# Kernel tuning notes

Measured on AMD Instinct MI355X. Metric: run time of the kernel, lower is better.

Reference implementation:

```python
import jax, jax.numpy as jnp
import numpy as np

L, E, TOP_K = 3, 8, 2
B, N, D, DS = 256, 1024, 512, 128

def setup_inputs() -> dict:
    key = jax.random.key(0)
    ks = jax.random.split(key, 10)
    s = 0.05  # weight init scale
    return {
        "token": jax.random.normal(ks[0], (B, 1, D), jnp.float32),
        "node_emb": jax.random.normal(ks[1], (B, N, D), jnp.float32),
        "states": jnp.zeros((L, E, B, DS), jnp.float32),
        "Wg": jax.random.normal(ks[2], (L, D, E), jnp.float32) * s,
        "bg": jnp.zeros((L, E), jnp.float32),
        "A": jax.random.normal(ks[3], (L, E, DS), jnp.float32),
        "Bin": jax.random.normal(ks[4], (L, E, D, DS), jnp.float32) * s,
        "Cout": jax.random.normal(ks[5], (L, E, DS, D), jnp.float32) * s,
        "Dsk": jax.random.normal(ks[6], (L, E, D), jnp.float32) * s,
        "Wq": jax.random.normal(ks[7], (D, D), jnp.float32) * s,
        "bq": jnp.zeros((D,), jnp.float32),
    }

def reference(token, node_emb, states, Wg, bg, A, Bin, Cout, Dsk, Wq, bq):
    # token: (B,1,D) -> h: (B,D)
    h = token[:, 0, :]
    lb_loss = jnp.float32(0.0)
    new_states = []
    for l in range(L):
        # --- MoE router: top-k softmax gating ---
        probs = jax.nn.softmax(h @ Wg[l] + bg[l])              # (B,E)
        topv, topi = jax.lax.top_k(probs, TOP_K)               # (B,k)
        gates_k = topv / jnp.sum(topv, axis=-1, keepdims=True)  # renormalized
        oh = jax.nn.one_hot(topi, E, dtype=probs.dtype)        # (B,k,E)
        gate_full = jnp.einsum('bk,bke->be', gates_k, oh)      # (B,E)
        sel = jnp.sum(oh, axis=1) > 0                          # (B,E) bool
        # --- state-space experts (computed densely for all experts) ---
        s = states[l]                                          # (E,B,DS)
        decay = jax.nn.sigmoid(A[l])[:, None, :]               # (E,1,DS)
        s_new = decay * s + jnp.einsum('bd,eds->ebs', h, Bin[l])   # (E,B,DS)
        y = jnp.einsum('ebs,esd->ebd', s_new, Cout[l]) + h[None] * Dsk[l][:, None, :]
        out = jnp.einsum('be,ebd->bd', gate_full, y)           # weighted combine
        # only routed experts advance their state
        keep = sel.T[:, :, None]                               # (E,B,1)
        new_states.append(jnp.where(keep, s_new, s))
        # load-balance loss: E * sum_e mean(probs_e) * mean(frac routed to e)
        lb_loss = lb_loss + E * jnp.sum(jnp.mean(probs, axis=0) * jnp.mean(sel.astype(probs.dtype), axis=0))
        h = h + out                                            # residual
    # --- query projection + logits over nodes ---
    q = h @ Wq + bq                                            # (B,D)
    logits = jnp.einsum('bd,bnd->bn', q, node_emb) / jnp.sqrt(jnp.float32(D))
    return logits, jnp.stack(new_states), lb_loss
```

## Files before the change

### kernel.cpp

```cpp
#include <hip/hip_runtime.h>
#include <math.h>

#define LNUM 3
#define ENUM 8
#define TOPK 2
#define BSZ 256
#define NSZ 1024
#define DSZ 512
#define SSZ 128

typedef float f32x4 __attribute__((ext_vector_type(4)));

__global__ __launch_bounds__(1024, 2) void fused_kernel(
    const float* __restrict__ token,
    const float* __restrict__ states,
    const float* __restrict__ Wg,
    const float* __restrict__ bg,
    const float* __restrict__ A,
    const float* __restrict__ Bin,
    const float* __restrict__ Cout,
    const float* __restrict__ Dsk,
    const float* __restrict__ Wq,
    const float* __restrict__ bq,
    float* __restrict__ out_states,
    float* __restrict__ acc,
    float* __restrict__ q_out)
{
    const int b = blockIdx.x;
    const int t = threadIdx.x;
    const int wave = t >> 6;
    const int lane = t & 63;
    const int ehalf = t >> 9;

    __shared__ float h_s[DSZ];
    __shared__ float snew_s[TOPK][SSZ];
    __shared__ float logit_s[ENUM];
    __shared__ f32x4 part4[1024];
    float* part = (float*)part4;

    if (t < DSZ) h_s[t] = token[b * DSZ + t];

    for (int l = 0; l < LNUM; ++l) {
        const float* Wg_l  = Wg  + (size_t)l * DSZ * ENUM;
        const float* bg_l  = bg  + (size_t)l * ENUM;
        const float* A_l   = A   + (size_t)l * ENUM * SSZ;
        const float* Bin_l = Bin + (size_t)l * ENUM * DSZ * SSZ;
        const float* Cou_l = Cout+ (size_t)l * ENUM * SSZ * DSZ;
        const float* Dsk_l = Dsk + (size_t)l * ENUM * DSZ;
        const float* st_l  = states     + (size_t)l * ENUM * BSZ * SSZ;
        float*       os_l  = out_states + (size_t)l * ENUM * BSZ * SSZ;

        __syncthreads();
        part4[t] = ((const f32x4*)Wg_l)[t];
        __syncthreads();

        if (wave < ENUM) {
            float p = 0.f;
            #pragma unroll
            for (int i = 0; i < 8; ++i) {
                const int d = lane + i * 64;
                p = fmaf(h_s[d], part[d * ENUM + wave], p);
            }
            for (int off = 32; off; off >>= 1) p += __shfl_down(p, off, 64);
            if (lane == 0) logit_s[wave] = p + bg_l[wave];
        }
        __syncthreads();

        float probs[ENUM];
        float mx = logit_s[0];
        for (int e = 1; e < ENUM; ++e) mx = fmaxf(mx, logit_s[e]);
        float ssum = 0.f;
        for (int e = 0; e < ENUM; ++e) { probs[e] = expf(logit_s[e] - mx); ssum += probs[e]; }
        const float sinv = 1.f / ssum;
        for (int e = 0; e < ENUM; ++e) probs[e] *= sinv;

        int i0 = 0;
        for (int e = 1; e < ENUM; ++e) if (probs[e] > probs[i0]) i0 = e;
        int i1 = -1;
        for (int e = 0; e < ENUM; ++e) {
            if (e == i0) continue;
            if (i1 < 0 || probs[e] > probs[i1]) i1 = e;
        }
        float g0 = probs[i0], g1 = probs[i1];
        const float ginv = 1.f / (g0 + g1);
        g0 *= ginv; g1 *= ginv;

        if (t < ENUM) {
            atomicAdd(&acc[(l * 2 + 0) * ENUM + t], probs[t]);
            atomicAdd(&acc[(l * 2 + 1) * ENUM + t], (t == i0 || t == i1) ? 1.0f : 0.0f);
        }
        const int esel = ehalf ? i1 : i0;

        {
            const int rem   = t & 511;
            const int c     = rem >> 5;
            const int squad = rem & 31;
            const float* Bp = Bin_l + (size_t)esel * DSZ * SSZ;
            const int d0 = c * 32;
            f32x4 acc4 = {0.f, 0.f, 0.f, 0.f};
            #pragma unroll
            for (int d = 0; d < 32; ++d)
                acc4 += *(const f32x4*)(Bp + (size_t)(d0 + d) * SSZ + squad * 4) * h_s[d0 + d];
            part4[(ehalf * 16 + c) * 32 + squad] = acc4;
        }
        __syncthreads();

        if (t < TOPK * SSZ) {
            const int k = t >> 7, s = t & 127;
            const int e = k ? i1 : i0;
            float sum = 0.f;
            #pragma unroll
            for (int c = 0; c < 16; ++c) sum += part[(k * 16 + c) * 128 + s];
            const float a = A_l[e * SSZ + s];
            const float decay = 1.f / (1.f + expf(-a));
            snew_s[k][s] = decay * st_l[((size_t)e * BSZ + b) * SSZ + s] + sum;
        }
        __syncthreads();

        {
            const int e = t >> 7, s = t & 127;
            float v;
            if (e == i0)      v = snew_s[0][s];
            else if (e == i1) v = snew_s[1][s];
            else              v = st_l[((size_t)e * BSZ + b) * SSZ + s];
            os_l[((size_t)e * BSZ + b) * SSZ + s] = v;
        }

        {
            const int rem   = t & 511;
            const int chunk = rem >> 7;
            const int dquad = rem & 127;
            const float* Cp = Cou_l + (size_t)esel * SSZ * DSZ;
            const float* sp = snew_s[ehalf];
            const int s0 = chunk * 32;
            f32x4 acc4 = {0.f, 0.f, 0.f, 0.f};
            #pragma unroll
            for (int s = 0; s < 32; ++s)
                acc4 += *(const f32x4*)(Cp + (size_t)(s0 + s) * DSZ + dquad * 4) * sp[s0 + s];
            part4[(ehalf * 4 + chunk) * 128 + dquad] = acc4;
        }
        __syncthreads();

        if (t < DSZ) {
            const float hd = h_s[t];
            float y0 = hd * Dsk_l[i0 * DSZ + t];
            float y1 = hd * Dsk_l[i1 * DSZ + t];
            #pragma unroll
            for (int c = 0; c < 4; ++c) {
                y0 += part[c * 512 + t];
                y1 += part[(4 + c) * 512 + t];
            }
            h_s[t] = hd + g0 * y0 + g1 * y1;
        }
    }

    __syncthreads();
    {
        const int chunk = t >> 7;
        const int dquad = t & 127;
        const int dd0 = chunk * 64;
        f32x4 acc4 = {0.f, 0.f, 0.f, 0.f};
        #pragma unroll 8
        for (int i = 0; i < 64; ++i)
            acc4 += *(const f32x4*)(Wq + (size_t)(dd0 + i) * DSZ + dquad * 4) * h_s[dd0 + i];
        part4[chunk * 128 + dquad] = acc4;
    }
    __syncthreads();
    if (t < DSZ) {
        float qv = bq[t];
        #pragma unroll
        for (int c = 0; c < 8; ++c) qv += part[c * 512 + t];
        q_out[b * DSZ + t] = qv;
    }
}

__global__ __launch_bounds__(256) void logits_kernel(
    const float* __restrict__ q, const float* __restrict__ node_emb,
    float* __restrict__ logits,
    const float* __restrict__ acc, float* __restrict__ loss_out)
{
    const int b = blockIdx.y;
    const int wave = threadIdx.x >> 6;
    const int lane = threadIdx.x & 63;

    if (blockIdx.x == 0 && blockIdx.y == 0 && threadIdx.x == 0) {
        float lb = 0.f;
        for (int l = 0; l < LNUM; ++l)
            for (int e = 0; e < ENUM; ++e) {
                const float mp = acc[(l * 2 + 0) * ENUM + e] * (1.0f / BSZ);
                const float ms = acc[(l * 2 + 1) * ENUM + e] * (1.0f / BSZ);
                lb += (float)ENUM * mp * ms;
            }
        loss_out[0] = lb;
    }

    const f32x4* q4 = (const f32x4*)(q + b * DSZ);
    const f32x4 q0 = q4[lane];
    const f32x4 q1 = q4[lane + 64];
    const float scale = 0.04419417382415922f;

    const int n0 = blockIdx.x * 128 + wave * 32;
    #pragma unroll 2
    for (int i = 0; i < 32; ++i) {
        const int n = n0 + i;
        const f32x4* r = (const f32x4*)(node_emb + ((size_t)b * NSZ + n) * DSZ);
        const f32x4 a0 = __builtin_nontemporal_load(&r[lane]);
        const f32x4 a1 = __builtin_nontemporal_load(&r[lane + 64]);
        float dot = a0.x * q0.x + a0.y * q0.y + a0.z * q0.z + a0.w * q0.w
                  + a1.x * q1.x + a1.y * q1.y + a1.z * q1.z + a1.w * q1.w;
        for (int off = 32; off; off >>= 1) dot += __shfl_down(dot, off, 64);
        if (lane == 0) logits[b * NSZ + n] = dot * scale;
    }
}

extern "C" void kernel_launch(void* const* d_in, const int* in_sizes, int n_in,
                              void* d_out, int out_size, void* d_ws, size_t ws_size,
                              hipStream_t stream) {
    const float* token    = (const float*)d_in[0];
    const float* node_emb = (const float*)d_in[1];
    const float* states   = (const float*)d_in[2];
    const float* Wg       = (const float*)d_in[3];
    const float* bg       = (const float*)d_in[4];
    const float* A        = (const float*)d_in[5];
    const float* Bin      = (const float*)d_in[6];
    const float* Cout     = (const float*)d_in[7];
    const float* Dsk      = (const float*)d_in[8];
    const float* Wq       = (const float*)d_in[9];
    const float* bq       = (const float*)d_in[10];

    float* out_logits = (float*)d_out;
    float* out_states = out_logits + (size_t)BSZ * NSZ;
    float* out_loss   = out_states + (size_t)LNUM * ENUM * BSZ * SSZ;

    float* ws_q   = (float*)d_ws;
    float* ws_acc = ws_q + (size_t)BSZ * DSZ;

    (void)hipMemsetAsync(ws_acc, 0, sizeof(float) * LNUM * 2 * ENUM, stream);

    fused_kernel<<<BSZ, 1024, 0, stream>>>(
        token, states, Wg, bg, A, Bin, Cout, Dsk, Wq, bq,
        out_states, ws_acc, ws_q);

    dim3 lg(NSZ / 128, BSZ);
    logits_kernel<<<lg, 256, 0, stream>>>(ws_q, node_emb, out_logits, ws_acc, out_loss);
}
```

Baseline: 172.5 us.

## Replace per-token fused MoE kernel with batched dense tiled GEMM pipeline

Replaces the single per-token fused kernel with a sequence of per-layer kernels. Each layer runs a split-K tiled shared-memory GEMM for the Bin projection over all experts and the whole batch, fused with the router, then a combine step that applies decay, gating and the state write. A second tiled GEMM handles Cout, and a final kernel does the residual update. The query projection becomes a split-K GEMM whose partials are reduced inside the logits kernel. The goal is to reuse expert weights across batch rows instead of re-streaming them once per token. The cost is computing all experts densely, extra workspace round-trips, and about 14 kernel launches.

After: 578.0 us. +235.1%, slower.

```diff
diff --git a/kernel.cpp b/kernel.cpp
--- a/kernel.cpp
+++ b/kernel.cpp
@@ -3,7 +3,6 @@
 
 #define LNUM 3
 #define ENUM 8
-#define TOPK 2
 #define BSZ 256
 #define NSZ 1024
 #define DSZ 512
@@ -11,201 +10,257 @@
 
 typedef float f32x4 __attribute__((ext_vector_type(4)));
 
-__global__ __launch_bounds__(1024, 2) void fused_kernel(
-    const float* __restrict__ token,
-    const float* __restrict__ states,
-    const float* __restrict__ Wg,
-    const float* __restrict__ bg,
-    const float* __restrict__ A,
-    const float* __restrict__ Bin,
-    const float* __restrict__ Cout,
-    const float* __restrict__ Dsk,
+template <int KC>
+__device__ __forceinline__ void gemm_tile(
+    const float* __restrict__ A, int lda,
+    const float* __restrict__ B, int ldb,
+    float* __restrict__ C, int ldc, int t)
+{
+    __shared__ float As[32][68];
+    __shared__ float Bs[32][128];
+
+    const int sx = t & 31;
+    const int ty = t >> 5;
+    const int brow = t >> 2;
+    const int kq = t & 3;
+    const int krow = t >> 3;
+    const int sq = t & 7;
+
+    f32x4 acc[8];
+    #pragma unroll
+    for (int r = 0; r < 8; ++r) acc[r] = (f32x4){0.f, 0.f, 0.f, 0.f};
+
+    for (int ks = 0; ks < KC; ks += 32) {
+        __syncthreads();
+        const f32x4 av0 = *(const f32x4*)(A + (size_t)brow * lda + ks + kq * 8);
+        const f32x4 av1 = *(const f32x4*)(A + (size_t)brow * lda + ks + kq * 8 + 4);
+        As[kq * 8 + 0][brow] = av0.x; As[kq * 8 + 1][brow] = av0.y;
+        As[kq * 8 + 2][brow] = av0.z; As[kq * 8 + 3][brow] = av0.w;
+        As[kq * 8 + 4][brow] = av1.x; As[kq * 8 + 5][brow] = av1.y;
+        As[kq * 8 + 6][brow] = av1.z; As[kq * 8 + 7][brow] = av1.w;
+        const float* Bp = B + (size_t)(ks + krow) * ldb + sq * 16;
+        *(f32x4*)&Bs[krow][sq * 16 + 0]  = *(const f32x4*)(Bp + 0);
+        *(f32x4*)&Bs[krow][sq * 16 + 4]  = *(const f32x4*)(Bp + 4);
+        *(f32x4*)&Bs[krow][sq * 16 + 8]  = *(const f32x4*)(Bp + 8);
+        *(f32x4*)&Bs[krow][sq * 16 + 12] = *(const f32x4*)(Bp + 12);
+        __syncthreads();
+
+        #pragma unroll
+        for (int k = 0; k < 32; ++k) {
+            const f32x4 a0 = *(const f32x4*)&As[k][ty * 8];
+            const f32x4 a1 = *(const f32x4*)&As[k][ty * 8 + 4];
+            const f32x4 bb = *(const f32x4*)&Bs[k][sx * 4];
+            acc[0] += bb * a0.x; acc[1] += bb * a0.y;
+            acc[2] += bb * a0.z; acc[3] += bb * a0.w;
+            acc[4] += bb * a1.x; acc[5] += bb * a1.y;
+            acc[6] += bb * a1.z; acc[7] += bb * a1.w;
+        }
+    }
+    #pragma unroll
+    for (int r = 0; r < 8; ++r)
+        *(f32x4*)(C + (size_t)(ty * 8 + r) * ldc + sx * 4) = acc[r];
+}
+
+__global__ __launch_bounds__(256) void k1_g1_gate(
+    const float* __restrict__ h,
+    const float* __restrict__ Bin_l,
+    const float* __restrict__ Wg_l,
+    const float* __restrict__ bg_l,
+    float* __restrict__ g1p,
+    float* __restrict__ gates,
+    float* __restrict__ acc_probs,
+    float* __restrict__ acc_sel)
+{
+    const int bid = blockIdx.x;
+    const int t = threadIdx.x;
+
+    if (bid < 256) {
+        const int kc = bid & 7;
+        const int bt = (bid >> 3) & 3;
+        const int e  = bid >> 5;
+        gemm_tile<64>(
+            h + (size_t)(bt * 64) * DSZ + kc * 64, DSZ,
+            Bin_l + (size_t)e * DSZ * SSZ + (size_t)(kc * 64) * SSZ, SSZ,
+            g1p + ((size_t)(kc * 8 + e) * BSZ + bt * 64) * SSZ, SSZ, t);
+        return;
+    }
+
+    __shared__ float lt[4][8];
+    const int wave = t >> 6, lane = t & 63;
+    const int e = lane >> 3, dg = lane & 7;
+    const int b0 = (bid - 256) * 64 + wave * 16;
+    for (int i = 0; i < 16; ++i) {
+        const int b = b0 + i;
+        float p = 0.f;
+        #pragma unroll 8
+        for (int j = 0; j < 64; ++j) {
+            const int d = dg + 8 * j;
+            p = fmaf(h[b * DSZ + d], Wg_l[d * ENUM + e], p);
+        }
+        p += __shfl_down(p, 4, 8);
+        p += __shfl_down(p, 2, 8);
+        p += __shfl_down(p, 1, 8);
+        if (dg == 0) lt[wave][e] = p + bg_l[e];
+        if (lane == 0) {
+            float probs[ENUM];
+            float mx = lt[wave][0];
+            for (int k = 1; k < ENUM; ++k) mx = fmaxf(mx, lt[wave][k]);
+            float ss = 0.f;
+            for (int k = 0; k < ENUM; ++k) { probs[k] = expf(lt[wave][k] - mx); ss += probs[k]; }
+            const float sinv = 1.f / ss;
+            for (int k = 0; k < ENUM; ++k) probs[k] *= sinv;
+            int i0 = 0;
+            for (int k = 1; k < ENUM; ++k) if (probs[k] > probs[i0]) i0 = k;
+            int i1 = -1;
+            for (int k = 0; k < ENUM; ++k) {
+                if (k == i0) continue;
+                if (i1 < 0 || probs[k] > probs[i1]) i1 = k;
+            }
+            const float gs = 1.f / (probs[i0] + probs[i1]);
+            for (int k = 0; k < ENUM; ++k) {
+                float g = 0.f;
+                if (k == i0) g = probs[i0] * gs;
+                else if (k == i1) g = probs[i1] * gs;
+                gates[b * ENUM + k] = g;
+                atomicAdd(&acc_probs[k], probs[k]);
+            }
+            atomicAdd(&acc_sel[i0], 1.0f);
+            atomicAdd(&acc_sel[i1], 1.0f);
+        }
+    }
+}
+
+__global__ __launch_bounds__(256) void k1b_combine(
+    const float* __restrict__ g1p,
+    const float* __restrict__ states_l,
+    const float* __restrict__ A_l,
+    const float* __restrict__ gates,
+    float* __restrict__ sng,
+    float* __restrict__ out_states_l)
+{
+    const int q = blockIdx.x * 256 + threadIdx.x;
+    const int e = q >> 13;
+    const int rem = q & 8191;
+    const int b = rem >> 5;
+    const int sq = rem & 31;
+
+    f32x4 sum = (f32x4){0.f, 0.f, 0.f, 0.f};
+    #pragma unroll
+    for (int kc = 0; kc < 8; ++kc)
+        sum += *(const f32x4*)(g1p + (size_t)kc * 262144 + (size_t)q * 4);
+
+    const f32x4 av = *(const f32x4*)(A_l + e * SSZ + sq * 4);
+    f32x4 decay;
+    decay.x = 1.f / (1.f + expf(-av.x));
+    decay.y = 1.f / (1.f + expf(-av.y));
+    decay.z = 1.f / (1.f + expf(-av.z));
+    decay.w = 1.f / (1.f + expf(-av.w));
+
+    const f32x4 stq = *(const f32x4*)(states_l + (size_t)q * 4);
+    const f32x4 snew = decay * stq + sum;
+    const float ge = gates[b * ENUM + e];
+
+    *(f32x4*)(sng + (size_t)q * 4) = snew * ge;
+    *(f32x4*)(out_states_l + (size_t)q * 4) = (ge > 0.f) ? snew : stq;
+}
+
+__global__ __launch_bounds__(256) void k2_g2(
+    const float* __restrict__ sng,
+    const float* __restrict__ Cout_l,
+    float* __restrict__ g2p)
+{
+    const int bid = blockIdx.x;
+    const int e  = bid & 7;
+    const int bt = (bid >> 3) & 3;
+    const int dt = bid >> 5;
+    gemm_tile<128>(
+        sng + (size_t)e * BSZ * SSZ + (size_t)(bt * 64) * SSZ, SSZ,
+        Cout_l + (size_t)e * SSZ * DSZ + dt * 128, DSZ,
+        g2p + ((size_t)e * BSZ + bt * 64) * DSZ + dt * 128, DSZ, threadIdx.x);
+}
+
+__global__ __launch_bounds__(256) void k3_hupd(
+    const float* __restrict__ h_in,
+    const float* __restrict__ g2p,
+    const float* __restrict__ Dsk_l,
+    const float* __restrict__ gates,
+    float* __restrict__ h_out)
+{
+    const int q = blockIdx.x * 256 + threadIdx.x;
+    const int b = q >> 7;
+    const int dq = q & 127;
+    const int d = dq * 4;
+
+    f32x4 acc = (f32x4){0.f, 0.f, 0.f, 0.f};
+    f32x4 dsum = (f32x4){0.f, 0.f, 0.f, 0.f};
+    #pragma unroll
+    for (int e = 0; e < ENUM; ++e) {
+        acc += *(const f32x4*)(g2p + ((size_t)e * BSZ + b) * DSZ + d);
+        dsum += *(const f32x4*)(Dsk_l + e * DSZ + d) * gates[b * ENUM + e];
+    }
+    const f32x4 hq = *(const f32x4*)(h_in + (size_t)b * DSZ + d);
+    *(f32x4*)(h_out + (size_t)b * DSZ + d) = hq + acc + hq * dsum;
+}
+
+__global__ __launch_bounds__(256) void k4_q(
+    const float* __restrict__ h,
     const float* __restrict__ Wq,
+    float* __restrict__ qp)
+{
+    const int bid = blockIdx.x;
+    const int kc = bid & 3;
+    const int bt = (bid >> 2) & 3;
+    const int dt = bid >> 4;
+    gemm_tile<128>(
+        h + (size_t)(bt * 64) * DSZ + kc * 128, DSZ,
+        Wq + (size_t)(kc * 128) * DSZ + dt * 128, DSZ,
+        qp + ((size_t)(kc * 256) + bt * 64) * DSZ + dt * 128, DSZ, threadIdx.x);
+}
+
+__global__ __launch_bounds__(256) void logits_kernel(
+    const float* __restrict__ qp,
     const float* __restrict__ bq,
-    float* __restrict__ out_states,
-    float* __restrict__ acc,
-    float* __restrict__ q_out)
-{
-    const int b = blockIdx.x;
-    const int t = threadIdx.x;
-    const int wave = t >> 6;
-    const int lane = t & 63;
-    const int ehalf = t >> 9;
-
-    __shared__ float h_s[DSZ];
-    __shared__ float snew_s[TOPK][SSZ];
-    __shared__ float logit_s[ENUM];
-    __shared__ f32x4 part4[1024];
-    float* part = (float*)part4;
-
-    if (t < DSZ) h_s[t] = token[b * DSZ + t];
-
-    for (int l = 0; l < LNUM; ++l) {
-        const float* Wg_l  = Wg  + (size_t)l * DSZ * ENUM;
-        const float* bg_l  = bg  + (size_t)l * ENUM;
-        const float* A_l   = A   + (size_t)l * ENUM * SSZ;
-        const float* Bin_l = Bin + (size_t)l * ENUM * DSZ * SSZ;
-        const float* Cou_l = Cout+ (size_t)l * ENUM * SSZ * DSZ;
-        const float* Dsk_l = Dsk + (size_t)l * ENUM * DSZ;
-        const float* st_l  = states     + (size_t)l * ENUM * BSZ * SSZ;
-        float*       os_l  = out_states + (size_t)l * ENUM * BSZ * SSZ;
-
-        __syncthreads();
-        part4[t] = ((const f32x4*)Wg_l)[t];
-        __syncthreads();
-
-        if (wave < ENUM) {
-            float p = 0.f;
-            #pragma unroll
-            for (int i = 0; i < 8; ++i) {
-                const int d = lane + i * 64;
-                p = fmaf(h_s[d], part[d * ENUM + wave], p);
-            }
-            for (int off = 32; off; off >>= 1) p += __shfl_down(p, off, 64);
-            if (lane == 0) logit_s[wave] = p + bg_l[wave];
-        }
-        __syncthreads();
-
-        float probs[ENUM];
-        float mx = logit_s[0];
-        for (int e = 1; e < ENUM; ++e) mx = fmaxf(mx, logit_s[e]);
-        float ssum = 0.f;
-        for (int e = 0; e < ENUM; ++e) { probs[e] = expf(logit_s[e] - mx); ssum += probs[e]; }
-        const float sinv = 1.f / ssum;
-        for (int e = 0; e < ENUM; ++e) probs[e] *= sinv;
-
-        int i0 = 0;
-        for (int e = 1; e < ENUM; ++e) if (probs[e] > probs[i0]) i0 = e;
-        int i1 = -1;
-        for (int e = 0; e < ENUM; ++e) {
-            if (e == i0) continue;
-            if (i1 < 0 || probs[e] > probs[i1]) i1 = e;
-        }
-        float g0 = probs[i0], g1 = probs[i1];
-        const float ginv = 1.f / (g0 + g1);
-        g0 *= ginv; g1 *= ginv;
-
-        if (t < ENUM) {
-            atomicAdd(&acc[(l * 2 + 0) * ENUM + t], probs[t]);
-            atomicAdd(&acc[(l * 2 + 1) * ENUM + t], (t == i0 || t == i1) ? 1.0f : 0.0f);
-        }
-        const int esel = ehalf ? i1 : i0;
-
-        {
-            const int rem   = t & 511;
-            const int c     = rem >> 5;
-            const int squad = rem & 31;
-            const float* Bp = Bin_l + (size_t)esel * DSZ * SSZ;
-            const int d0 = c * 32;
-            f32x4 acc4 = {0.f, 0.f, 0.f, 0.f};
-            #pragma unroll
-            for (int d = 0; d < 32; ++d)
-                acc4 += *(const f32x4*)(Bp + (size_t)(d0 + d) * SSZ + squad * 4) * h_s[d0 + d];
-            part4[(ehalf * 16 + c) * 32 + squad] = acc4;
-        }
-        __syncthreads();
-
-        if (t < TOPK * SSZ) {
-            const int k = t >> 7, s = t & 127;
-            const int e = k ? i1 : i0;
-            float sum = 0.f;
-            #pragma unroll
-            for (int c = 0; c < 16; ++c) sum += part[(k * 16 + c) * 128 + s];
-            const float a = A_l[e * SSZ + s];
-            const float decay = 1.f / (1.f + expf(-a));
-            snew_s[k][s] = decay * st_l[((size_t)e * BSZ + b) * SSZ + s] + sum;
-        }
-        __syncthreads();
-
-        {
-            const int e = t >> 7, s = t & 127;
-            float v;
-            if (e == i0)      v = snew_s[0][s];
-            else if (e == i1) v = snew_s[1][s];
-            else              v = st_l[((size_t)e * BSZ + b) * SSZ + s];
-            os_l[((size_t)e * BSZ + b) * SSZ + s] = v;
-        }
-
-        {
-            const int rem   = t & 511;
-            const int chunk = rem >> 7;
-            const int dquad = rem & 127;
-            const float* Cp = Cou_l + (size_t)esel * SSZ * DSZ;
-            const float* sp = snew_s[ehalf];
-            const int s0 = chunk * 32;
-            f32x4 acc4 = {0.f, 0.f, 0.f, 0.f};
-            #pragma unroll
-            for (int s = 0; s < 32; ++s)
-                acc4 += *(const f32x4*)(Cp + (size_t)(s0 + s) * DSZ + dquad * 4) * sp[s0 + s];
-            part4[(ehalf * 4 + chunk) * 128 + dquad] = acc4;
-        }
-        __syncthreads();
-
-        if (t < DSZ) {
-            const float hd = h_s[t];
-            float y0 = hd * Dsk_l[i0 * DSZ + t];
-            float y1 = hd * Dsk_l[i1 * DSZ + t];
-            #pragma unroll
-            for (int c = 0; c < 4; ++c) {
-                y0 += part[c * 512 + t];
-                y1 += part[(4 + c) * 512 + t];
-            }
-            h_s[t] = hd + g0 * y0 + g1 * y1;
-        }
-    }
-
-    __syncthreads();
-    {
-        const int chunk = t >> 7;
-        const int dquad = t & 127;
-        const int dd0 = chunk * 64;
-        f32x4 acc4 = {0.f, 0.f, 0.f, 0.f};
-        #pragma unroll 8
-        for (int i = 0; i < 64; ++i)
-            acc4 += *(const f32x4*)(Wq + (size_t)(dd0 + i) * DSZ + dquad * 4) * h_s[dd0 + i];
-        part4[chunk * 128 + dquad] = acc4;
-    }
-    __syncthreads();
-    if (t < DSZ) {
-        float qv = bq[t];
-        #pragma unroll
-        for (int c = 0; c < 8; ++c) qv += part[c * 512 + t];
-        q_out[b * DSZ + t] = qv;
-    }
-}
-
-__global__ __launch_bounds__(256) void logits_kernel(
-    const float* __restrict__ q, const float* __restrict__ node_emb,
+    const float* __restrict__ node_emb,
     float* __restrict__ logits,
     const float* __restrict__ acc, float* __restrict__ loss_out)
 {
     const int b = blockIdx.y;
     const int wave = threadIdx.x >> 6;
     const int lane = threadIdx.x & 63;
+
+    __shared__ float q_s[DSZ];
+    if (threadIdx.x < 128) {
+        const int d = threadIdx.x * 4;
+        f32x4 qv = *(const f32x4*)(bq + d);
+        #pragma unroll
+        for (int kc = 0; kc < 4; ++kc)
+            qv += *(const f32x4*)(qp + ((size_t)(kc * 256) + b) * DSZ + d);
+        *(f32x4*)&q_s[d] = qv;
+    }
+    __syncthreads();
 
     if (blockIdx.x == 0 && blockIdx.y == 0 && threadIdx.x == 0) {
         float lb = 0.f;
         for (int l = 0; l < LNUM; ++l)
             for (int e = 0; e < ENUM; ++e) {
-                const float mp = acc[(l * 2 + 0) * ENUM + e] * (1.0f / BSZ);
-                const float ms = acc[(l * 2 + 1) * ENUM + e] * (1.0f / BSZ);
+                const float mp = acc[l * 16 + e] * (1.0f / BSZ);
+                const float ms = acc[l * 16 + 8 + e] * (1.0f / BSZ);
                 lb += (float)ENUM * mp * ms;
             }
         loss_out[0] = lb;
     }
 
-    const f32x4* q4 = (const f32x4*)(q + b * DSZ);
-    const f32x4 q0 = q4[lane];
-    const f32x4 q1 = q4[lane + 64];
+    const f32x4 q0 = *(const f32x4*)&q_s[lane * 4];
+    const f32x4 q1 = *(const f32x4*)&q_s[256 + lane * 4];
     const float scale = 0.04419417382415922f;
 
     const int n0 = blockIdx.x * 128 + wave * 32;
     #pragma unroll 2
     for (int i = 0; i < 32; ++i) {
         const int n = n0 + i;
-        const f32x4* r = (const f32x4*)(node_emb + ((size_t)b * NSZ + n) * DSZ);
-        const f32x4 a0 = __builtin_nontemporal_load(&r[lane]);
-        const f32x4 a1 = __builtin_nontemporal_load(&r[lane + 64]);
+        const float* r = node_emb + ((size_t)b * NSZ + n) * DSZ;
+        const f32x4 a0 = __builtin_nontemporal_load((const f32x4*)(r) + lane);
+        const f32x4 a1 = __builtin_nontemporal_load((const f32x4*)(r) + lane + 64);
         float dot = a0.x * q0.x + a0.y * q0.y + a0.z * q0.z + a0.w * q0.w
                   + a1.x * q1.x + a1.y * q1.y + a1.z * q1.z + a1.w * q1.w;
         for (int off = 32; off; off >>= 1) dot += __shfl_down(dot, off, 64);
@@ -232,15 +287,41 @@
     float* out_states = out_logits + (size_t)BSZ * NSZ;
     float* out_loss   = out_states + (size_t)LNUM * ENUM * BSZ * SSZ;
 
-    float* ws_q   = (float*)d_ws;
-    float* ws_acc = ws_q + (size_t)BSZ * DSZ;
-
-    (void)hipMemsetAsync(ws_acc, 0, sizeof(float) * LNUM * 2 * ENUM, stream);
-
-    fused_kernel<<<BSZ, 1024, 0, stream>>>(
-        token, states, Wg, bg, A, Bin, Cout, Dsk, Wq, bq,
-        out_states, ws_acc, ws_q);
+    float* ws_g1p   = (float*)d_ws;
+    float* ws_g2p   = ws_g1p + 2097152;
+    float* ws_qp    = ws_g2p + 1048576;
+    float* ws_sng   = ws_qp  + 524288;
+    float* ws_h     = ws_sng + 262144;
+    float* ws_gates = ws_h   + 131072;
+    float* ws_acc   = ws_gates + 2048;
+
+    (void)hipMemsetAsync(ws_acc, 0, sizeof(float) * LNUM * 16, stream);
+
+    const float* h_cur = token;
+    for (int l = 0; l < LNUM; ++l) {
+        const float* Bin_l = Bin + (size_t)l * ENUM * DSZ * SSZ;
+        const float* Cou_l = Cout + (size_t)l * ENUM * SSZ * DSZ;
+        const float* st_l  = states + (size_t)l * ENUM * BSZ * SSZ;
+        float* os_l        = out_states + (size_t)l * ENUM * BSZ * SSZ;
+
+        k1_g1_gate<<<260, 256, 0, stream>>>(
+            h_cur, Bin_l,
+            Wg + (size_t)l * DSZ * ENUM, bg + (size_t)l * ENUM,
+            ws_g1p, ws_gates, ws_acc + l * 16, ws_acc + l * 16 + 8);
+
+        k1b_combine<<<256, 256, 0, stream>>>(
+            ws_g1p, st_l, A + (size_t)l * ENUM * SSZ, ws_gates, ws_sng, os_l);
+
+        k2_g2<<<128, 256, 0, stream>>>(ws_sng, Cou_l, ws_g2p);
+
+        k3_hupd<<<128, 256, 0, stream>>>(
+            h_cur, ws_g2p, Dsk + (size_t)l * ENUM * DSZ, ws_gates, ws_h);
+
+        h_cur = ws_h;
+    }
+
+    k4_q<<<64, 256, 0, stream>>>(ws_h, Wq, ws_qp);
 
     dim3 lg(NSZ / 128, BSZ);
-    logits_kernel<<<lg, 256, 0, stream>>>(ws_q, node_emb, out_logits, ws_acc, out_loss);
-}
+    logits_kernel<<<lg, 256, 0, stream>>>(ws_qp, bq, node_emb, out_logits, ws_acc, out_loss);
+}
```

## Split fused per-batch kernel into per-layer kernels with one block per expert slot

Applied to the files above, without the earlier changes.

Replaces the single 1024-thread fused kernel that looped over all layers with one launch per layer. Each launch uses 512 blocks of 512 threads, one block per (batch row, top-k slot), and passes the residual stream through global workspace buffers. The Wq projection becomes its own kernel split across two column halves. The goal is more blocks and better occupancy during the memory-bound expert matvecs. The cost is extra launches, recomputing the router in both blocks of a pair, and global round-trips for h and y.

New measurement: 184.2 us. +6.8%, slower.

```diff
diff --git a/kernel.cpp b/kernel.cpp
--- a/kernel.cpp
+++ b/kernel.cpp
@@ -3,7 +3,6 @@
 
 #define LNUM 3
 #define ENUM 8
-#define TOPK 2
 #define BSZ 256
 #define NSZ 1024
 #define DSZ 512
@@ -11,166 +10,174 @@
 
 typedef float f32x4 __attribute__((ext_vector_type(4)));
 
-__global__ __launch_bounds__(1024, 2) void fused_kernel(
-    const float* __restrict__ token,
-    const float* __restrict__ states,
-    const float* __restrict__ Wg,
-    const float* __restrict__ bg,
-    const float* __restrict__ A,
-    const float* __restrict__ Bin,
-    const float* __restrict__ Cout,
-    const float* __restrict__ Dsk,
-    const float* __restrict__ Wq,
-    const float* __restrict__ bq,
-    float* __restrict__ out_states,
-    float* __restrict__ acc,
-    float* __restrict__ q_out)
+__global__ __launch_bounds__(512, 4) void layer2_kernel(
+    const float* __restrict__ h_base,
+    const float* __restrict__ y_in,
+    float* __restrict__ h_store,
+    float* __restrict__ y_out,
+    const float* __restrict__ Wg_l,
+    const float* __restrict__ bg_l,
+    const float* __restrict__ A_l,
+    const float* __restrict__ Bin_l,
+    const float* __restrict__ Cou_l,
+    const float* __restrict__ Dsk_l,
+    const float* __restrict__ st_l,
+    float* __restrict__ os_l,
+    float* __restrict__ acc_probs,
+    float* __restrict__ acc_sel)
 {
-    const int b = blockIdx.x;
+    const int b = blockIdx.x & 255;
+    const int k = blockIdx.x >> 8;
     const int t = threadIdx.x;
     const int wave = t >> 6;
     const int lane = t & 63;
-    const int ehalf = t >> 9;
 
     __shared__ float h_s[DSZ];
-    __shared__ float snew_s[TOPK][SSZ];
+    __shared__ float snew_s[SSZ];
     __shared__ float logit_s[ENUM];
-    __shared__ f32x4 part4[1024];
+    __shared__ f32x4 part4[512];
     float* part = (float*)part4;
 
-    if (t < DSZ) h_s[t] = token[b * DSZ + t];
-
-    for (int l = 0; l < LNUM; ++l) {
-        const float* Wg_l  = Wg  + (size_t)l * DSZ * ENUM;
-        const float* bg_l  = bg  + (size_t)l * ENUM;
-        const float* A_l   = A   + (size_t)l * ENUM * SSZ;
-        const float* Bin_l = Bin + (size_t)l * ENUM * DSZ * SSZ;
-        const float* Cou_l = Cout+ (size_t)l * ENUM * SSZ * DSZ;
-        const float* Dsk_l = Dsk + (size_t)l * ENUM * DSZ;
-        const float* st_l  = states     + (size_t)l * ENUM * BSZ * SSZ;
-        float*       os_l  = out_states + (size_t)l * ENUM * BSZ * SSZ;
-
-        __syncthreads();
-        part4[t] = ((const f32x4*)Wg_l)[t];
-        __syncthreads();
-
-        if (wave < ENUM) {
-            float p = 0.f;
-            #pragma unroll
-            for (int i = 0; i < 8; ++i) {
-                const int d = lane + i * 64;
-                p = fmaf(h_s[d], part[d * ENUM + wave], p);
-            }
-            for (int off = 32; off; off >>= 1) p += __shfl_down(p, off, 64);
-            if (lane == 0) logit_s[wave] = p + bg_l[wave];
+    if (t < 128) {
+        f32x4 hq = ((const f32x4*)(h_base + (size_t)b * DSZ))[t];
+        if (y_in) {
+            hq += ((const f32x4*)(y_in + (size_t)b * DSZ))[t];
+            hq += ((const f32x4*)(y_in + (size_t)(BSZ + b) * DSZ))[t];
         }
-        __syncthreads();
-
-        float probs[ENUM];
-        float mx = logit_s[0];
-        for (int e = 1; e < ENUM; ++e) mx = fmaxf(mx, logit_s[e]);
-        float ssum = 0.f;
-        for (int e = 0; e < ENUM; ++e) { probs[e] = expf(logit_s[e] - mx); ssum += probs[e]; }
-        const float sinv = 1.f / ssum;
-        for (int e = 0; e < ENUM; ++e) probs[e] *= sinv;
-
-        int i0 = 0;
-        for (int e = 1; e < ENUM; ++e) if (probs[e] > probs[i0]) i0 = e;
-        int i1 = -1;
-        for (int e = 0; e < ENUM; ++e) {
-            if (e == i0) continue;
-            if (i1 < 0 || probs[e] > probs[i1]) i1 = e;
+        ((f32x4*)h_s)[t] = hq;
+        if (h_store && k == 0) ((f32x4*)(h_store + (size_t)b * DSZ))[t] = hq;
+    }
+    __syncthreads();
+
+    {
+        float p = 0.f;
+        #pragma unroll
+        for (int i = 0; i < 8; ++i) {
+            const int d = lane + i * 64;
+            p = fmaf(h_s[d], Wg_l[d * ENUM + wave], p);
         }
-        float g0 = probs[i0], g1 = probs[i1];
-        const float ginv = 1.f / (g0 + g1);
-        g0 *= ginv; g1 *= ginv;
-
-        if (t < ENUM) {
-            atomicAdd(&acc[(l * 2 + 0) * ENUM + t], probs[t]);
-            atomicAdd(&acc[(l * 2 + 1) * ENUM + t], (t == i0 || t == i1) ? 1.0f : 0.0f);
-        }
-        const int esel = ehalf ? i1 : i0;
-
-        {
-            const int rem   = t & 511;
-            const int c     = rem >> 5;
-            const int squad = rem & 31;
-            const float* Bp = Bin_l + (size_t)esel * DSZ * SSZ;
-            const int d0 = c * 32;
-            f32x4 acc4 = {0.f, 0.f, 0.f, 0.f};
-            #pragma unroll
-            for (int d = 0; d < 32; ++d)
-                acc4 += *(const f32x4*)(Bp + (size_t)(d0 + d) * SSZ + squad * 4) * h_s[d0 + d];
-            part4[(ehalf * 16 + c) * 32 + squad] = acc4;
-        }
-        __syncthreads();
-
-        if (t < TOPK * SSZ) {
-            const int k = t >> 7, s = t & 127;
-            const int e = k ? i1 : i0;
-            float sum = 0.f;
-            #pragma unroll
-            for (int c = 0; c < 16; ++c) sum += part[(k * 16 + c) * 128 + s];
-            const float a = A_l[e * SSZ + s];
-            const float decay = 1.f / (1.f + expf(-a));
-            snew_s[k][s] = decay * st_l[((size_t)e * BSZ + b) * SSZ + s] + sum;
-        }
-        __syncthreads();
-
-        {
-            const int e = t >> 7, s = t & 127;
-            float v;
-            if (e == i0)      v = snew_s[0][s];
-            else if (e == i1) v = snew_s[1][s];
-            else              v = st_l[((size_t)e * BSZ + b) * SSZ + s];
-            os_l[((size_t)e * BSZ + b) * SSZ + s] = v;
-        }
-
-        {
-            const int rem   = t & 511;
-            const int chunk = rem >> 7;
-            const int dquad = rem & 127;
-            const float* Cp = Cou_l + (size_t)esel * SSZ * DSZ;
-            const float* sp = snew_s[ehalf];
-            const int s0 = chunk * 32;
-            f32x4 acc4 = {0.f, 0.f, 0.f, 0.f};
-            #pragma unroll
-            for (int s = 0; s < 32; ++s)
-                acc4 += *(const f32x4*)(Cp + (size_t)(s0 + s) * DSZ + dquad * 4) * sp[s0 + s];
-            part4[(ehalf * 4 + chunk) * 128 + dquad] = acc4;
-        }
-        __syncthreads();
-
-        if (t < DSZ) {
-            const float hd = h_s[t];
-            float y0 = hd * Dsk_l[i0 * DSZ + t];
-            float y1 = hd * Dsk_l[i1 * DSZ + t];
-            #pragma unroll
-            for (int c = 0; c < 4; ++c) {
-                y0 += part[c * 512 + t];
-                y1 += part[(4 + c) * 512 + t];
-            }
-            h_s[t] = hd + g0 * y0 + g1 * y1;
-        }
-    }
-
-    __syncthreads();
-    {
-        const int chunk = t >> 7;
-        const int dquad = t & 127;
-        const int dd0 = chunk * 64;
-        f32x4 acc4 = {0.f, 0.f, 0.f, 0.f};
-        #pragma unroll 8
+        for (int off = 32; off; off >>= 1) p += __shfl_down(p, off, 64);
+        if (lane == 0) logit_s[wave] = p + bg_l[wave];
+    }
+    __syncthreads();
+
+    float probs[ENUM];
+    float mx = logit_s[0];
+    for (int e = 1; e < ENUM; ++e) mx = fmaxf(mx, logit_s[e]);
+    float ssum = 0.f;
+    for (int e = 0; e < ENUM; ++e) { probs[e] = expf(logit_s[e] - mx); ssum += probs[e]; }
+    const float sinv = 1.f / ssum;
+    for (int e = 0; e < ENUM; ++e) probs[e] *= sinv;
+
+    int i0 = 0;
+    for (int e = 1; e < ENUM; ++e) if (probs[e] > probs[i0]) i0 = e;
+    int i1 = -1;
+    for (int e = 0; e < ENUM; ++e) {
+        if (e == i0) continue;
+        if (i1 < 0 || probs[e] > probs[i1]) i1 = e;
+    }
+    float g0 = probs[i0], g1 = probs[i1];
+    const float ginv = 1.f / (g0 + g1);
+    g0 *= ginv; g1 *= ginv;
+
+    if (k == 0 && t < ENUM) {
+        atomicAdd(&acc_probs[t], probs[t]);
+        atomicAdd(&acc_sel[t], (t == i0 || t == i1) ? 1.0f : 0.0f);
+    }
+
+    const int esel = k ? i1 : i0;
+    const float gsel = k ? g1 : g0;
+
+    {
+        const int kc = t >> 5, sq = t & 31;
+        const float* Bp = Bin_l + (size_t)esel * DSZ * SSZ + sq * 4;
+        const int d0 = kc * 32;
+        f32x4 a4 = {0.f, 0.f, 0.f, 0.f};
+        #pragma unroll
+        for (int d = 0; d < 32; ++d)
+            a4 += *(const f32x4*)(Bp + (size_t)(d0 + d) * SSZ) * h_s[d0 + d];
+        part4[t] = a4;
+    }
+    __syncthreads();
+
+    if (t < SSZ) {
+        float sum = 0.f;
+        #pragma unroll
+        for (int kc = 0; kc < 16; ++kc) sum += part[kc * 128 + t];
+        const float a = A_l[esel * SSZ + t];
+        const float decay = 1.f / (1.f + expf(-a));
+        snew_s[t] = decay * st_l[((size_t)esel * BSZ + b) * SSZ + t] + sum;
+    }
+    __syncthreads();
+
+    if (t < SSZ) os_l[((size_t)esel * BSZ + b) * SSZ + t] = snew_s[t];
+    {
+        const int e = k * 4 + (t >> 7);
+        const int s = t & 127;
+        if (e != i0 && e != i1)
+            os_l[((size_t)e * BSZ + b) * SSZ + s] = st_l[((size_t)e * BSZ + b) * SSZ + s];
+    }
+
+    {
+        const int sc = t >> 7, dq = t & 127;
+        const float* Cp = Cou_l + (size_t)esel * SSZ * DSZ + dq * 4;
+        const int s0 = sc * 32;
+        f32x4 a4 = {0.f, 0.f, 0.f, 0.f};
+        #pragma unroll
+        for (int s = 0; s < 32; ++s)
+            a4 += *(const f32x4*)(Cp + (size_t)(s0 + s) * DSZ) * snew_s[s0 + s];
+        part4[sc * 128 + dq] = a4;
+    }
+    __syncthreads();
+
+    if (t < 128) {
+        f32x4 yq = part4[t] + part4[128 + t] + part4[256 + t] + part4[384 + t];
+        const f32x4 hq = ((const f32x4*)h_s)[t];
+        const f32x4 dk = *(const f32x4*)(Dsk_l + esel * DSZ + t * 4);
+        yq += hq * dk;
+        ((f32x4*)(y_out + (size_t)(k * BSZ + b) * DSZ))[t] = yq * gsel;
+    }
+}
+
+__global__ __launch_bounds__(512, 4) void q2_kernel(
+    const float* __restrict__ h_base,
+    const float* __restrict__ y_in,
+    const float* __restrict__ Wq,
+    const float* __restrict__ bq,
+    float* __restrict__ q_out)
+{
+    const int b = blockIdx.x & 255;
+    const int k = blockIdx.x >> 8;
+    const int t = threadIdx.x;
+
+    __shared__ float h_s[DSZ];
+    __shared__ f32x4 part4[512];
+
+    if (t < 128) {
+        f32x4 hq = ((const f32x4*)(h_base + (size_t)b * DSZ))[t]
+                 + ((const f32x4*)(y_in + (size_t)b * DSZ))[t]
+                 + ((const f32x4*)(y_in + (size_t)(BSZ + b) * DSZ))[t];
+        ((f32x4*)h_s)[t] = hq;
+    }
+    __syncthreads();
+
+    {
+        const int kc = t >> 6, cq = t & 63;
+        const float* Wp = Wq + k * 256 + cq * 4;
+        const int d0 = kc * 64;
+        f32x4 a4 = {0.f, 0.f, 0.f, 0.f};
+        #pragma unroll
         for (int i = 0; i < 64; ++i)
-            acc4 += *(const f32x4*)(Wq + (size_t)(dd0 + i) * DSZ + dquad * 4) * h_s[dd0 + i];
-        part4[chunk * 128 + dquad] = acc4;
-    }
-    __syncthreads();
-    if (t < DSZ) {
-        float qv = bq[t];
-        #pragma unroll
-        for (int c = 0; c < 8; ++c) qv += part[c * 512 + t];
-        q_out[b * DSZ + t] = qv;
+            a4 += *(const f32x4*)(Wp + (size_t)(d0 + i) * DSZ) * h_s[d0 + i];
+        part4[kc * 64 + cq] = a4;
+    }
+    __syncthreads();
+
+    if (t < 64) {
+        f32x4 qq = *(const f32x4*)(bq + k * 256 + t * 4);
+        #pragma unroll
+        for (int kc = 0; kc < 8; ++kc) qq += part4[kc * 64 + t];
+        ((f32x4*)(q_out + (size_t)b * DSZ))[k * 64 + t] = qq;
     }
 }
 
@@ -234,12 +241,34 @@
 
     float* ws_q   = (float*)d_ws;
     float* ws_acc = ws_q + (size_t)BSZ * DSZ;
-
-    (void)hipMemsetAsync(ws_acc, 0, sizeof(float) * LNUM * 2 * ENUM, stream);
-
-    fused_kernel<<<BSZ, 1024, 0, stream>>>(
-        token, states, Wg, bg, A, Bin, Cout, Dsk, Wq, bq,
-        out_states, ws_acc, ws_q);
+    float* hbuf0  = ws_acc + 64;
+    float* hbuf1  = hbuf0 + (size_t)BSZ * DSZ;
+    float* ybufA  = hbuf1 + (size_t)BSZ * DSZ;
+    float* ybufB  = ybufA + (size_t)2 * BSZ * DSZ;
+
+    (void)hipMemsetAsync(ws_acc, 0, sizeof(float) * LNUM * 16, stream);
+
+    const float* y_ins[LNUM]   = { nullptr, ybufA, ybufB };
+    float*       h_stores[LNUM]= { nullptr, hbuf0, hbuf1 };
+    float*       y_outs[LNUM]  = { ybufA,   ybufB, ybufA };
+    const float* h_bases[LNUM] = { token,   token, hbuf0 };
+
+    for (int l = 0; l < LNUM; ++l) {
+        layer2_kernel<<<512, 512, 0, stream>>>(
+            h_bases[l], y_ins[l], h_stores[l], y_outs[l],
+            Wg  + (size_t)l * DSZ * ENUM,
+            bg  + (size_t)l * ENUM,
+            A   + (size_t)l * ENUM * SSZ,
+            Bin + (size_t)l * ENUM * DSZ * SSZ,
+            Cout+ (size_t)l * ENUM * SSZ * DSZ,
+            Dsk + (size_t)l * ENUM * DSZ,
+            states + (size_t)l * ENUM * BSZ * SSZ,
+            out_states + (size_t)l * ENUM * BSZ * SSZ,
+            ws_acc + (l * 2 + 0) * ENUM,
+            ws_acc + (l * 2 + 1) * ENUM);
+    }
+
+    q2_kernel<<<512, 512, 0, stream>>>(hbuf1, ybufA, Wq, bq, ws_q);
 
     dim3 lg(NSZ / 128, BSZ);
     logits_kernel<<<lg, 256, 0, stream>>>(ws_q, node_emb, out_logits, ws_acc, out_loss);
```
